# Kernel tuning notes

Measured on AMD Instinct MI355X. Metric: run time of the kernel, lower is better.

The kernel has to match this reference:

```python
import jax, jax.numpy as jnp
import numpy as np

MARGIN = 0.2
NEG_SENTINEL = -1e30


def setup_inputs() -> dict:
    key = jax.random.key(0)
    k1, k2 = jax.random.split(key)
    batch_reprs = jax.random.normal(k1, (4096, 128), dtype=jnp.float32)
    batch_labels = jax.random.randint(k2, (4096,), 0, 512, dtype=jnp.int64 if jax.config.jax_enable_x64 else jnp.int32)
    return {"batch_reprs": batch_reprs, "batch_labels": batch_labels}


def _loss(batch_reprs, batch_labels):
    # class match matrix (self-similarity kept, as in original)
    match = (batch_labels[:, None] == batch_labels[None, :]).astype(batch_reprs.dtype)  # [B,B]

    # pairwise euclidean distance (squared=False), sim = -dist
    sq = jnp.sum(batch_reprs * batch_reprs, axis=1)
    d2 = jnp.maximum(sq[:, None] + sq[None, :] - 2.0 * (batch_reprs @ batch_reprs.T), 0.0)
    zero = (d2 == 0.0).astype(batch_reprs.dtype)
    dist = jnp.sqrt(d2 + zero * 1e-16) * (1.0 - zero)
    sim_hat = -dist + (1.0 - match) * MARGIN  # use_margin=True

    # rank positions via double argsort (descending)
    order = jnp.argsort(-sim_hat, axis=1)
    rank = jnp.argsort(order, axis=1).astype(sim_hat.dtype) + 1.0  # [B,B], 1-based ranks

    k = jnp.sum(match, axis=1, keepdims=True)                      # n_pos per row, [B,1]
    fp = (match < 1.0) & (rank <= k)                               # false positives
    fp_num = jnp.sum(fp, axis=1, keepdims=True).astype(sim_hat.dtype)
    fn = (match > 0.0) & (rank > k)                                # false negatives

    n = sim_hat.shape[1]
    # per-row top-(fp_num) false negatives by sim_hat, vectorized via masked sort
    fn_scores = jnp.where(fn, sim_hat, NEG_SENTINEL)
    idx = jnp.argsort(-fn_scores, axis=1)
    fn_sorted = jnp.take_along_axis(sim_hat, idx, axis=1)
    fn_ranks = jnp.take_along_axis(rank, idx, axis=1)
    fn_mask_sorted = jnp.take_along_axis(fn, idx, axis=1)
    sel = (jnp.arange(n)[None, :] < fp_num) & fn_mask_sorted       # top fp_num entries

    # weighted margins (rows with fp_num==0 contribute 0 automatically)
    fp_term = jnp.sum(jnp.where(fp, sim_hat * (0.5 + (k - rank + 1.0) / k * 0.5), 0.0))
    fn_term = jnp.sum(jnp.where(sel, fn_sorted * (0.5 + (fn_ranks - k) / (n - k) * 0.5), 0.0))
    return fp_term - fn_term


def reference(batch_reprs, batch_labels):
    return _loss(batch_reprs, batch_labels)
```

## Files before the change

### kernel.cpp

```cpp
#include <hip/hip_runtime.h>
#include <cstdint>
#include <cstddef>

#define B 4096
#define D 128
#define MARGIN_F 0.2f
#define CW 256

typedef short bf16x8 __attribute__((ext_vector_type(8)));
typedef float f32x4 __attribute__((ext_vector_type(4)));

__device__ __forceinline__ uint32_t xform_key(float f) {
    uint32_t u = __float_as_uint(f);
    return u ^ (uint32_t)((((int32_t)u) >> 31) | 0x80000000);
}
__device__ __forceinline__ float unxform16(uint32_t k16) {
    uint32_t u = k16 << 16;
    u = (u & 0x80000000u) ? (u ^ 0x80000000u) : ~u;
    return __uint_as_float(u);
}
__device__ __forceinline__ unsigned short f2bf(float f) {
    uint32_t u = __float_as_uint(f);
    return (unsigned short)((u + 0x7FFFu + ((u >> 16) & 1u)) >> 16);
}

__global__ __launch_bounds__(256) void sq_kernel(const float* __restrict__ R,
                                                 float* __restrict__ sq,
                                                 float* __restrict__ out) {
    if (blockIdx.x == 0 && threadIdx.x == 0) out[0] = 0.0f;
    int wave = threadIdx.x >> 6;
    int lane = threadIdx.x & 63;
    int row  = blockIdx.x * 4 + wave;
    const float2* R2 = (const float2*)R + (size_t)row * (D / 2);
    float2 v = R2[lane];
    float s = v.x * v.x + v.y * v.y;
#pragma unroll
    for (int off = 32; off > 0; off >>= 1) s += __shfl_down(s, off);
    if (lane == 0) sq[row] = s;
}

__global__ __launch_bounds__(256) void conv_kernel(const float* __restrict__ R,
                                                   unsigned short* __restrict__ Rb) {
    int idx = (blockIdx.x * 256 + threadIdx.x) * 4;
    float4 v = *(const float4*)(R + idx);
    ushort4 o;
    o.x = f2bf(v.x); o.y = f2bf(v.y); o.z = f2bf(v.z); o.w = f2bf(v.w);
    *(ushort4*)(Rb + idx) = o;
}

__global__ __launch_bounds__(256) void gemm_sim_mfma(const unsigned short* __restrict__ Rb,
                                                     const float* __restrict__ sq,
                                                     const int* __restrict__ labels,
                                                     unsigned short* __restrict__ simk) {
    __shared__ unsigned short sAB[32768];

    const int tid  = threadIdx.x;
    const int wid  = tid >> 6, lane = tid & 63;
    const int q    = lane >> 4, t = lane & 15;
    const int Ay0  = blockIdx.y * 128;
    const int Bx0  = blockIdx.x * 128;
    const int m0   = (wid >> 1) * 64;
    const int n0   = (wid & 1) * 64;

#pragma unroll
    for (int it = 0; it < 16; ++it) {
        int s = (wid * 16 + it) * 64 + lane;
        int local = s & 2047;
        int r = local >> 4;
        int p = local & 15;
        int srcrow = ((s < 2048) ? Ay0 : Bx0) + r;
        const uint4* src = (const uint4*)(Rb + (size_t)srcrow * D + ((p ^ (r & 15)) << 3));
        *(uint4*)(&sAB[(size_t)s * 8]) = *src;
    }
    __syncthreads();

    f32x4 acc[4][4];
#pragma unroll
    for (int mi = 0; mi < 4; ++mi)
#pragma unroll
        for (int ni = 0; ni < 4; ++ni) acc[mi][ni] = (f32x4)0.0f;

#pragma unroll
    for (int kq = 0; kq < 4; ++kq) {
        bf16x8 af[4], bfr[4];
        const int ksw = (kq * 4 + q);
#pragma unroll
        for (int mi = 0; mi < 4; ++mi) {
            int r = m0 + mi * 16 + t;
            af[mi] = *(bf16x8*)(&sAB[(size_t)r * 128 + ((ksw ^ t) << 3)]);
        }
#pragma unroll
        for (int ni = 0; ni < 4; ++ni) {
            int r = n0 + ni * 16 + t;
            bfr[ni] = *(bf16x8*)(&sAB[16384 + (size_t)r * 128 + ((ksw ^ t) << 3)]);
        }
#pragma unroll
        for (int mi = 0; mi < 4; ++mi)
#pragma unroll
            for (int ni = 0; ni < 4; ++ni)
                acc[mi][ni] = __builtin_amdgcn_mfma_f32_16x16x32_bf16(
                    af[mi], bfr[ni], acc[mi][ni], 0, 0, 0);
    }

    __syncthreads();

    const int epi0 = wid * 4608;
    float sqc[4]; int lc[4];
#pragma unroll
    for (int ni = 0; ni < 4; ++ni) {
        sqc[ni] = sq[Bx0 + n0 + ni * 16 + t];
        lc[ni]  = labels[Bx0 + n0 + ni * 16 + t];
    }
#pragma unroll
    for (int mi = 0; mi < 4; ++mi) {
#pragma unroll
        for (int r = 0; r < 4; ++r) {
            int lrow = mi * 16 + q * 4 + r;
            int grow = Ay0 + m0 + lrow;
            float sqr = sq[grow];
            int   lr  = labels[grow];
#pragma unroll
            for (int ni = 0; ni < 4; ++ni) {
                float g  = acc[mi][ni][r];
                float d2 = fmaxf(sqr + sqc[ni] - 2.0f * g, 0.0f);
                float dist = (d2 > 0.0f) ? sqrtf(d2) : 0.0f;
                float s = -dist + ((lr == lc[ni]) ? 0.0f : MARGIN_F);
                uint32_t key = xform_key(s);
                sAB[epi0 + lrow * 72 + ni * 16 + t] =
                    (unsigned short)((key + 0x8000u) >> 16);
            }
        }
    }
#pragma unroll
    for (int it = 0; it < 8; ++it) {
        int rr = it * 8 + (lane >> 3);
        int cc = (lane & 7) * 8;
        uint4 v = *(uint4*)(&sAB[epi0 + rr * 72 + cc]);
        *(uint4*)(simk + (size_t)(Ay0 + m0 + rr) * B + Bx0 + n0 + cc) = v;
    }
}

__global__ __launch_bounds__(256) void row_loss16(const unsigned short* __restrict__ simk,
                                                  const int* __restrict__ labels,
                                                  float* __restrict__ out) {
    __shared__ uint32_t cand_u[4][CW];
    __shared__ int      cand_m[4][CW];
    __shared__ int      cnt_w[4];
    __shared__ float    wsum[4];

    const int wid  = threadIdx.x >> 6;
    const int lane = threadIdx.x & 63;
    const int row  = blockIdx.x * 4 + wid;

    if (lane == 0) cnt_w[wid] = 0;

    const uint4* pv = (const uint4*)(simk + (size_t)row * B);
    const int4*  lv = (const int4*)labels;
    const int li = labels[row];

    uint4 kv[8];
    uint64_t mbits = 0;
    uint32_t t1 = 0, t2 = 0;
#pragma unroll
    for (int q = 0; q < 8; ++q) {
        kv[q] = pv[q * 64 + lane];
        const int lb = (q * 64 + lane) * 2;
        int4 la = lv[lb], lc = lv[lb + 1];
        uint32_t u[8] = {kv[q].x & 0xFFFFu, kv[q].x >> 16,
                         kv[q].y & 0xFFFFu, kv[q].y >> 16,
                         kv[q].z & 0xFFFFu, kv[q].z >> 16,
                         kv[q].w & 0xFFFFu, kv[q].w >> 16};
#pragma unroll
        for (int c = 0; c < 8; ++c) {
            uint32_t mn = min(t1, u[c]);
            t1 = max(t1, u[c]);
            t2 = max(t2, mn);
        }
        mbits |= (uint64_t)(la.x == li) << (q * 8 + 0);
        mbits |= (uint64_t)(la.y == li) << (q * 8 + 1);
        mbits |= (uint64_t)(la.z == li) << (q * 8 + 2);
        mbits |= (uint64_t)(la.w == li) << (q * 8 + 3);
        mbits |= (uint64_t)(lc.x == li) << (q * 8 + 4);
        mbits |= (uint64_t)(lc.y == li) << (q * 8 + 5);
        mbits |= (uint64_t)(lc.z == li) << (q * 8 + 6);
        mbits |= (uint64_t)(lc.w == li) << (q * 8 + 7);
    }

    int kloc = __popcll(mbits);
#pragma unroll
    for (int off = 32; off > 0; off >>= 1) kloc += __shfl_xor(kloc, off);
    const int k = kloc;
    const float kf = (float)k;

    const int kneed = min(k, 128);
    uint32_t T = 0;
#pragma unroll
    for (int b = 15; b >= 0; --b) {
        uint32_t g = T | (1u << b);
        int c = __popcll(__ballot(t1 >= g)) + __popcll(__ballot(t2 >= g));
        if (c >= kneed) T = g;
    }

#pragma unroll
    for (int q = 0; q < 8; ++q) {
        uint32_t u[8] = {kv[q].x & 0xFFFFu, kv[q].x >> 16,
                         kv[q].y & 0xFFFFu, kv[q].y >> 16,
                         kv[q].z & 0xFFFFu, kv[q].z >> 16,
                         kv[q].w & 0xFFFFu, kv[q].w >> 16};
#pragma unroll
        for (int c = 0; c < 8; ++c) {
            int e = q * 8 + c;
            int m = (int)((mbits >> e) & 1);
            if (u[c] >= T || m) {
                int p = atomicAdd(&cnt_w[wid], 1);
                if (p < CW) {
                    cand_u[wid][p] = u[c];
                    cand_m[wid][p] = ((q * 64 + lane) * 8 + c) | (m << 12);
                }
            }
        }
    }
    const int ncand = min(cnt_w[wid], CW);

    float facc = 0.0f;

    for (int s = lane; s < ncand; s += 64) {
        uint32_t uc = cand_u[wid][s];
        int meta = cand_m[wid][s];
        int jc = meta & 0xFFF;
        int m  = (meta >> 12) & 1;
        if (uc >= T) {
            int cnt = 0;
            for (int c = 0; c < ncand; ++c) {
                uint32_t u2 = cand_u[wid][c];
                int j2 = cand_m[wid][c] & 0xFFF;
                cnt += (u2 > uc || (u2 == uc && j2 < jc)) ? 1 : 0;
            }
            int rank = 1 + cnt;
            float v = unxform16(uc);
            if (!m && rank <= k)
                facc += v * (0.5f + ((kf - (float)rank + 1.0f) / kf) * 0.5f);
            else if (m && rank > k)
                facc -= v * (0.5f + (((float)rank - kf) / (float)(B - k)) * 0.5f);
        }
    }

    for (int c = 0; c < ncand; ++c) {
        uint32_t uc = cand_u[wid][c];
        if (uc < T) {
            int jc = cand_m[wid][c] & 0xFFF;
            int cnt = 0;
#pragma unroll
            for (int q = 0; q < 8; ++q) {
                uint32_t u[8] = {kv[q].x & 0xFFFFu, kv[q].x >> 16,
                                 kv[q].y & 0xFFFFu, kv[q].y >> 16,
                                 kv[q].z & 0xFFFFu, kv[q].z >> 16,
                                 kv[q].w & 0xFFFFu, kv[q].w >> 16};
                int jb = (q * 64 + lane) * 8;
#pragma unroll
                for (int cc = 0; cc < 8; ++cc)
                    cnt += (u[cc] > uc || (u[cc] == uc && jb + cc < jc)) ? 1 : 0;
            }
#pragma unroll
            for (int off = 32; off > 0; off >>= 1) cnt += __shfl_xor(cnt, off);
            if (lane == 0) {
                int rank = 1 + cnt;
                float v = unxform16(uc);
                facc -= v * (0.5f + (((float)rank - kf) / (float)(B - k)) * 0.5f);
            }
        }
    }

#pragma unroll
    for (int off = 32; off > 0; off >>= 1) facc += __shfl_xor(facc, off);
    if (lane == 0) wsum[wid] = facc;
    __syncthreads();
    if (threadIdx.x == 0)
        atomicAdd(out, wsum[0] + wsum[1] + wsum[2] + wsum[3]);
}

extern "C" void kernel_launch(void* const* d_in, const int* in_sizes, int n_in,
                              void* d_out, int out_size, void* d_ws, size_t ws_size,
                              hipStream_t stream) {
    const float* R      = (const float*)d_in[0];
    const int*   labels = (const int*)d_in[1];
    float* out = (float*)d_out;

    float*          sq   = (float*)d_ws;
    unsigned short* Rb   = (unsigned short*)((char*)d_ws + 16 * 1024);
    unsigned short* simk = (unsigned short*)((char*)d_ws + 16 * 1024 + 1024 * 1024 + 256);

    hipLaunchKernelGGL(sq_kernel, dim3(B / 4), dim3(256), 0, stream, R, sq, out);
    hipLaunchKernelGGL(conv_kernel, dim3(B * D / 1024), dim3(256), 0, stream, R, Rb);
    hipLaunchKernelGGL(gemm_sim_mfma, dim3(B / 128, B / 128), dim3(256), 0, stream,
                       Rb, sq, labels, simk);
    hipLaunchKernelGGL(row_loss16, dim3(B / 4), dim3(256), 0, stream, simk, labels, out);
}
```

Before: 147.5 us.

## Load GEMM fragments from global directly; pack rank keys and batch FN rank counting

The GEMM kernel stops staging A/B tiles in shared memory and has each lane read its MFMA fragments straight from global/L2, keeping LDS only for the epilogue. The row-loss kernel moves to one 64-thread block per row and packs value and index tie-break into a single 32-bit key, which shortens the candidate-rank comparisons. Below-threshold false negatives are ranked four at a time over the register-held row, so there are fewer cross-lane reductions. In exchange, the GEMM reads uncoalesced, redundant fragments from global memory, and single-wave blocks drop the block-level sync but launch many more workgroups.

```diff
diff --git a/kernel.cpp b/kernel.cpp
--- a/kernel.cpp
+++ b/kernel.cpp
@@ -48,11 +48,11 @@
     *(ushort4*)(Rb + idx) = o;
 }
 
-__global__ __launch_bounds__(256) void gemm_sim_mfma(const unsigned short* __restrict__ Rb,
-                                                     const float* __restrict__ sq,
-                                                     const int* __restrict__ labels,
-                                                     unsigned short* __restrict__ simk) {
-    __shared__ unsigned short sAB[32768];
+__global__ __launch_bounds__(256) void gemm_sim_v3(const unsigned short* __restrict__ Rb,
+                                                   const float* __restrict__ sq,
+                                                   const int* __restrict__ labels,
+                                                   unsigned short* __restrict__ simk) {
+    __shared__ unsigned short sEP[4][4608];
 
     const int tid  = threadIdx.x;
     const int wid  = tid >> 6, lane = tid & 63;
@@ -62,38 +62,24 @@
     const int m0   = (wid >> 1) * 64;
     const int n0   = (wid & 1) * 64;
 
-#pragma unroll
-    for (int it = 0; it < 16; ++it) {
-        int s = (wid * 16 + it) * 64 + lane;
-        int local = s & 2047;
-        int r = local >> 4;
-        int p = local & 15;
-        int srcrow = ((s < 2048) ? Ay0 : Bx0) + r;
-        const uint4* src = (const uint4*)(Rb + (size_t)srcrow * D + ((p ^ (r & 15)) << 3));
-        *(uint4*)(&sAB[(size_t)s * 8]) = *src;
-    }
-    __syncthreads();
-
     f32x4 acc[4][4];
 #pragma unroll
     for (int mi = 0; mi < 4; ++mi)
 #pragma unroll
         for (int ni = 0; ni < 4; ++ni) acc[mi][ni] = (f32x4)0.0f;
+
+    const unsigned short* baseA = Rb + (size_t)(Ay0 + m0 + t) * D + q * 8;
+    const unsigned short* baseB = Rb + (size_t)(Bx0 + n0 + t) * D + q * 8;
 
 #pragma unroll
     for (int kq = 0; kq < 4; ++kq) {
         bf16x8 af[4], bfr[4];
-        const int ksw = (kq * 4 + q);
-#pragma unroll
-        for (int mi = 0; mi < 4; ++mi) {
-            int r = m0 + mi * 16 + t;
-            af[mi] = *(bf16x8*)(&sAB[(size_t)r * 128 + ((ksw ^ t) << 3)]);
-        }
-#pragma unroll
-        for (int ni = 0; ni < 4; ++ni) {
-            int r = n0 + ni * 16 + t;
-            bfr[ni] = *(bf16x8*)(&sAB[16384 + (size_t)r * 128 + ((ksw ^ t) << 3)]);
-        }
+#pragma unroll
+        for (int mi = 0; mi < 4; ++mi)
+            af[mi] = *(const bf16x8*)(baseA + (size_t)mi * 16 * D + kq * 32);
+#pragma unroll
+        for (int ni = 0; ni < 4; ++ni)
+            bfr[ni] = *(const bf16x8*)(baseB + (size_t)ni * 16 * D + kq * 32);
 #pragma unroll
         for (int mi = 0; mi < 4; ++mi)
 #pragma unroll
@@ -102,9 +88,6 @@
                     af[mi], bfr[ni], acc[mi][ni], 0, 0, 0);
     }
 
-    __syncthreads();
-
-    const int epi0 = wid * 4608;
     float sqc[4]; int lc[4];
 #pragma unroll
     for (int ni = 0; ni < 4; ++ni) {
@@ -126,7 +109,7 @@
                 float dist = (d2 > 0.0f) ? sqrtf(d2) : 0.0f;
                 float s = -dist + ((lr == lc[ni]) ? 0.0f : MARGIN_F);
                 uint32_t key = xform_key(s);
-                sAB[epi0 + lrow * 72 + ni * 16 + t] =
+                sEP[wid][lrow * 72 + ni * 16 + t] =
                     (unsigned short)((key + 0x8000u) >> 16);
             }
         }
@@ -135,24 +118,20 @@
     for (int it = 0; it < 8; ++it) {
         int rr = it * 8 + (lane >> 3);
         int cc = (lane & 7) * 8;
-        uint4 v = *(uint4*)(&sAB[epi0 + rr * 72 + cc]);
+        uint4 v = *(uint4*)(&sEP[wid][rr * 72 + cc]);
         *(uint4*)(simk + (size_t)(Ay0 + m0 + rr) * B + Bx0 + n0 + cc) = v;
     }
 }
 
-__global__ __launch_bounds__(256) void row_loss16(const unsigned short* __restrict__ simk,
-                                                  const int* __restrict__ labels,
-                                                  float* __restrict__ out) {
-    __shared__ uint32_t cand_u[4][CW];
-    __shared__ int      cand_m[4][CW];
-    __shared__ int      cnt_w[4];
-    __shared__ float    wsum[4];
-
-    const int wid  = threadIdx.x >> 6;
-    const int lane = threadIdx.x & 63;
-    const int row  = blockIdx.x * 4 + wid;
-
-    if (lane == 0) cnt_w[wid] = 0;
+__global__ __launch_bounds__(64, 4) void row_loss_w64(const unsigned short* __restrict__ simk,
+                                                      const int* __restrict__ labels,
+                                                      float* __restrict__ out) {
+    __shared__ uint32_t cand_c[CW];
+    __shared__ int cnt;
+
+    const int lane = threadIdx.x;
+    const int row  = blockIdx.x;
+    if (lane == 0) cnt = 0;
 
     const uint4* pv = (const uint4*)(simk + (size_t)row * B);
     const int4*  lv = (const int4*)labels;
@@ -200,6 +179,7 @@
         int c = __popcll(__ballot(t1 >= g)) + __popcll(__ballot(t2 >= g));
         if (c >= kneed) T = g;
     }
+    const uint32_t combT = T << 12;
 
 #pragma unroll
     for (int q = 0; q < 8; ++q) {
@@ -207,37 +187,32 @@
                          kv[q].y & 0xFFFFu, kv[q].y >> 16,
                          kv[q].z & 0xFFFFu, kv[q].z >> 16,
                          kv[q].w & 0xFFFFu, kv[q].w >> 16};
+        int jb = (q * 64 + lane) * 8;
 #pragma unroll
         for (int c = 0; c < 8; ++c) {
             int e = q * 8 + c;
-            int m = (int)((mbits >> e) & 1);
+            uint32_t m = (uint32_t)((mbits >> e) & 1);
             if (u[c] >= T || m) {
-                int p = atomicAdd(&cnt_w[wid], 1);
-                if (p < CW) {
-                    cand_u[wid][p] = u[c];
-                    cand_m[wid][p] = ((q * 64 + lane) * 8 + c) | (m << 12);
-                }
-            }
-        }
-    }
-    const int ncand = min(cnt_w[wid], CW);
+                int p = atomicAdd(&cnt, 1);
+                if (p < CW)
+                    cand_c[p] = (u[c] << 12) | (uint32_t)(4095 - (jb + c)) | (m << 31);
+            }
+        }
+    }
+    const int ncand = min(cnt, CW);
 
     float facc = 0.0f;
 
     for (int s = lane; s < ncand; s += 64) {
-        uint32_t uc = cand_u[wid][s];
-        int meta = cand_m[wid][s];
-        int jc = meta & 0xFFF;
-        int m  = (meta >> 12) & 1;
-        if (uc >= T) {
-            int cnt = 0;
-            for (int c = 0; c < ncand; ++c) {
-                uint32_t u2 = cand_u[wid][c];
-                int j2 = cand_m[wid][c] & 0xFFF;
-                cnt += (u2 > uc || (u2 == uc && j2 < jc)) ? 1 : 0;
-            }
-            int rank = 1 + cnt;
-            float v = unxform16(uc);
+        uint32_t cs = cand_c[s];
+        uint32_t comb = cs & 0x7FFFFFFFu;
+        int m = (int)(cs >> 31);
+        if (comb >= combT) {
+            int c2 = 0;
+            for (int c = 0; c < ncand; ++c)
+                c2 += ((cand_c[c] & 0x7FFFFFFFu) > comb) ? 1 : 0;
+            int rank = 1 + c2;
+            float v = unxform16(comb >> 12);
             if (!m && rank <= k)
                 facc += v * (0.5f + ((kf - (float)rank + 1.0f) / kf) * 0.5f);
             else if (m && rank > k)
@@ -245,11 +220,22 @@
         }
     }
 
-    for (int c = 0; c < ncand; ++c) {
-        uint32_t uc = cand_u[wid][c];
-        if (uc < T) {
-            int jc = cand_m[wid][c] & 0xFFF;
-            int cnt = 0;
+    uint32_t p0 = 0xFFFFFFFFu, p1 = 0xFFFFFFFFu, p2 = 0xFFFFFFFFu, p3 = 0xFFFFFFFFu;
+    int np = 0;
+    for (int c = 0; c <= ncand; ++c) {
+        bool flushit = (c == ncand);
+        if (!flushit) {
+            uint32_t cc_ = cand_c[c];
+            if ((cc_ & 0x80000000u) && (cc_ & 0x7FFFFFFFu) < combT) {
+                uint32_t comb = cc_ & 0x7FFFFFFFu;
+                if (np == 0) p0 = comb; else if (np == 1) p1 = comb;
+                else if (np == 2) p2 = comb; else p3 = comb;
+                ++np;
+                flushit = (np == 4);
+            }
+        }
+        if (flushit && np > 0) {
+            int c0 = 0, c1 = 0, c2 = 0, c3 = 0;
 #pragma unroll
             for (int q = 0; q < 8; ++q) {
                 uint32_t u[8] = {kv[q].x & 0xFFFFu, kv[q].x >> 16,
@@ -258,25 +244,35 @@
                                  kv[q].w & 0xFFFFu, kv[q].w >> 16};
                 int jb = (q * 64 + lane) * 8;
 #pragma unroll
-                for (int cc = 0; cc < 8; ++cc)
-                    cnt += (u[cc] > uc || (u[cc] == uc && jb + cc < jc)) ? 1 : 0;
-            }
-#pragma unroll
-            for (int off = 32; off > 0; off >>= 1) cnt += __shfl_xor(cnt, off);
+                for (int cc = 0; cc < 8; ++cc) {
+                    uint32_t comb_e = (u[cc] << 12) | (uint32_t)(4095 - (jb + cc));
+                    c0 += (comb_e > p0) ? 1 : 0;
+                    c1 += (comb_e > p1) ? 1 : 0;
+                    c2 += (comb_e > p2) ? 1 : 0;
+                    c3 += (comb_e > p3) ? 1 : 0;
+                }
+            }
+#pragma unroll
+            for (int off = 32; off > 0; off >>= 1) {
+                c0 += __shfl_xor(c0, off); c1 += __shfl_xor(c1, off);
+                c2 += __shfl_xor(c2, off); c3 += __shfl_xor(c3, off);
+            }
             if (lane == 0) {
-                int rank = 1 + cnt;
-                float v = unxform16(uc);
-                facc -= v * (0.5f + (((float)rank - kf) / (float)(B - k)) * 0.5f);
-            }
+                int rk[4] = {1 + c0, 1 + c1, 1 + c2, 1 + c3};
+                uint32_t pp[4] = {p0, p1, p2, p3};
+                for (int i = 0; i < np; ++i) {
+                    float v = unxform16(pp[i] >> 12);
+                    facc -= v * (0.5f + (((float)rk[i] - kf) / (float)(B - k)) * 0.5f);
+                }
+            }
+            p0 = p1 = p2 = p3 = 0xFFFFFFFFu;
+            np = 0;
         }
     }
 
 #pragma unroll
     for (int off = 32; off > 0; off >>= 1) facc += __shfl_xor(facc, off);
-    if (lane == 0) wsum[wid] = facc;
-    __syncthreads();
-    if (threadIdx.x == 0)
-        atomicAdd(out, wsum[0] + wsum[1] + wsum[2] + wsum[3]);
+    if (lane == 0) atomicAdd(out, facc);
 }
 
 extern "C" void kernel_launch(void* const* d_in, const int* in_sizes, int n_in,
@@ -292,7 +288,7 @@
 
     hipLaunchKernelGGL(sq_kernel, dim3(B / 4), dim3(256), 0, stream, R, sq, out);
     hipLaunchKernelGGL(conv_kernel, dim3(B * D / 1024), dim3(256), 0, stream, R, Rb);
-    hipLaunchKernelGGL(gemm_sim_mfma, dim3(B / 128, B / 128), dim3(256), 0, stream,
+    hipLaunchKernelGGL(gemm_sim_v3, dim3(B / 128, B / 128), dim3(256), 0, stream,
                        Rb, sq, labels, simk);
-    hipLaunchKernelGGL(row_loss16, dim3(B / 4), dim3(256), 0, stream, simk, labels, out);
-}
+    hipLaunchKernelGGL(row_loss_w64, dim3(B), dim3(64), 0, stream, simk, labels, out);
+}
```

Result: slower. 158.6 us (+7.5%).

## Fuse bf16 conversion into sq kernel and remap block order for L2 locality

Applied to the files above, without the earlier changes.

The separate fp32-to-bf16 conversion kernel is merged into the squared-norm kernel, which saves one launch and one read of the input. The GEMM grid is flattened so that consecutive blocks walk down the row tiles within one column tile. The row-loss blocks are remapped to rows in a matching pattern, so the loss kernel tends to read similarity rows soon after the GEMM wrote them and while they may still be in cache. The remapping changes the order of float atomic adds, which can slightly change the result through rounding.

```diff
diff --git a/kernel.cpp b/kernel.cpp
--- a/kernel.cpp
+++ b/kernel.cpp
@@ -9,6 +9,7 @@
 
 typedef short bf16x8 __attribute__((ext_vector_type(8)));
 typedef float f32x4 __attribute__((ext_vector_type(4)));
+typedef uint32_t u32x4 __attribute__((ext_vector_type(4)));
 
 __device__ __forceinline__ uint32_t xform_key(float f) {
     uint32_t u = __float_as_uint(f);
@@ -24,28 +25,22 @@
     return (unsigned short)((u + 0x7FFFu + ((u >> 16) & 1u)) >> 16);
 }
 
-__global__ __launch_bounds__(256) void sq_kernel(const float* __restrict__ R,
-                                                 float* __restrict__ sq,
-                                                 float* __restrict__ out) {
+__global__ __launch_bounds__(256) void prep_kernel(const float* __restrict__ R,
+                                                   float* __restrict__ sq,
+                                                   unsigned short* __restrict__ Rb,
+                                                   float* __restrict__ out) {
     if (blockIdx.x == 0 && threadIdx.x == 0) out[0] = 0.0f;
     int wave = threadIdx.x >> 6;
     int lane = threadIdx.x & 63;
     int row  = blockIdx.x * 4 + wave;
     const float2* R2 = (const float2*)R + (size_t)row * (D / 2);
     float2 v = R2[lane];
+    ushort2 o; o.x = f2bf(v.x); o.y = f2bf(v.y);
+    *(ushort2*)(Rb + (size_t)row * D + lane * 2) = o;
     float s = v.x * v.x + v.y * v.y;
 #pragma unroll
     for (int off = 32; off > 0; off >>= 1) s += __shfl_down(s, off);
     if (lane == 0) sq[row] = s;
-}
-
-__global__ __launch_bounds__(256) void conv_kernel(const float* __restrict__ R,
-                                                   unsigned short* __restrict__ Rb) {
-    int idx = (blockIdx.x * 256 + threadIdx.x) * 4;
-    float4 v = *(const float4*)(R + idx);
-    ushort4 o;
-    o.x = f2bf(v.x); o.y = f2bf(v.y); o.z = f2bf(v.z); o.w = f2bf(v.w);
-    *(ushort4*)(Rb + idx) = o;
 }
 
 __global__ __launch_bounds__(256) void gemm_sim_mfma(const unsigned short* __restrict__ Rb,
@@ -54,11 +49,12 @@
                                                      unsigned short* __restrict__ simk) {
     __shared__ unsigned short sAB[32768];
 
+    const int id   = blockIdx.x;
+    const int Ay0  = (id % 32) * 128;
+    const int Bx0  = (id / 32) * 128;
     const int tid  = threadIdx.x;
     const int wid  = tid >> 6, lane = tid & 63;
     const int q    = lane >> 4, t = lane & 15;
-    const int Ay0  = blockIdx.y * 128;
-    const int Bx0  = blockIdx.x * 128;
     const int m0   = (wid >> 1) * 64;
     const int n0   = (wid & 1) * 64;
 
@@ -150,7 +146,9 @@
 
     const int wid  = threadIdx.x >> 6;
     const int lane = threadIdx.x & 63;
-    const int row  = blockIdx.x * 4 + wid;
+    const int x    = blockIdx.x & 7;
+    const int g    = blockIdx.x >> 3;
+    const int row  = (x + 8 * (g >> 5)) * 128 + ((g & 31) * 4 + wid);
 
     if (lane == 0) cnt_w[wid] = 0;
 
@@ -196,9 +194,9 @@
     uint32_t T = 0;
 #pragma unroll
     for (int b = 15; b >= 0; --b) {
-        uint32_t g = T | (1u << b);
-        int c = __popcll(__ballot(t1 >= g)) + __popcll(__ballot(t2 >= g));
-        if (c >= kneed) T = g;
+        uint32_t g2 = T | (1u << b);
+        int c = __popcll(__ballot(t1 >= g2)) + __popcll(__ballot(t2 >= g2));
+        if (c >= kneed) T = g2;
     }
 
 #pragma unroll
@@ -290,9 +288,8 @@
     unsigned short* Rb   = (unsigned short*)((char*)d_ws + 16 * 1024);
     unsigned short* simk = (unsigned short*)((char*)d_ws + 16 * 1024 + 1024 * 1024 + 256);
 
-    hipLaunchKernelGGL(sq_kernel, dim3(B / 4), dim3(256), 0, stream, R, sq, out);
-    hipLaunchKernelGGL(conv_kernel, dim3(B * D / 1024), dim3(256), 0, stream, R, Rb);
-    hipLaunchKernelGGL(gemm_sim_mfma, dim3(B / 128, B / 128), dim3(256), 0, stream,
+    hipLaunchKernelGGL(prep_kernel, dim3(B / 4), dim3(256), 0, stream, R, sq, Rb, out);
+    hipLaunchKernelGGL(gemm_sim_mfma, dim3(1024), dim3(256), 0, stream,
                        Rb, sq, labels, simk);
-    hipLaunchKernelGGL(row_loss16, dim3(B / 4), dim3(256), 0, stream, simk, labels, out);
-}
+    hipLaunchKernelGGL(row_loss16, dim3(1024), dim3(256), 0, stream, simk, labels, out);
+}
```

New measurement: 150.0 us. No clear change (+1.7%).
